# Performance work log

Hardware: AMD Instinct MI355X
Metric: run time of the kernel (lower is better)

Reference implementation:

```python
import jax, jax.numpy as jnp
import numpy as np

ALPHA = 1.0
BETA = 1.0


def setup_inputs() -> dict:
    key = jax.random.key(0)
    k1, k2, k3, k4 = jax.random.split(key, 4)
    B_, S, D_in, D_out, R = 4, 64, 8192, 8192, 16
    x = jax.random.normal(k1, (B_, S, D_in), dtype=jnp.float32)
    original_weight = jax.random.normal(k2, (D_out, D_in), dtype=jnp.float32) * 0.02
    A = jax.random.normal(k3, (D_out, R), dtype=jnp.float32) * 0.02
    Bm = jax.random.normal(k4, (R, D_in), dtype=jnp.float32) * 0.02
    return {"x": x, "original_weight": original_weight, "A": A, "B": Bm}


def reference(x, original_weight, A, B):
    # delta_weight = alpha * (A @ B)  -> [D_out, D_in]
    delta_weight = ALPHA * jnp.matmul(A, B)
    # F.linear(x, W + beta*delta) = x @ (W + beta*delta)^T
    W = original_weight + BETA * delta_weight
    return jnp.einsum("bsd,od->bso", x, W)
```

## Files before the change

kernel.cpp:

```cpp
#include <hip/hip_runtime.h>
#include <stdint.h>


#define DM 256
#define DK 8192
#define DN 8192
#define RLORA 16

#define TN 64
#define BK 64
#define KSPLIT 4
#define KCHUNK (DK / KSPLIT)
#define NITER (KCHUNK / BK)

typedef short bf16x8 __attribute__((ext_vector_type(8)));
typedef float f32x4v __attribute__((ext_vector_type(4)));

__device__ __forceinline__ unsigned short f2bf(float f) {
  unsigned u = __builtin_bit_cast(unsigned, f);
  u += 0x7FFFu + ((u >> 16) & 1u);
  return (unsigned short)(u >> 16);
}

__device__ __forceinline__ bf16x8 pack8(float4 a, float4 b) {
  bf16x8 r;
  r[0] = (short)f2bf(a.x); r[1] = (short)f2bf(a.y);
  r[2] = (short)f2bf(a.z); r[3] = (short)f2bf(a.w);
  r[4] = (short)f2bf(b.x); r[5] = (short)f2bf(b.y);
  r[6] = (short)f2bf(b.z); r[7] = (short)f2bf(b.w);
  return r;
}

__global__ __launch_bounds__(256) void prep_x(
    const float* __restrict__ x, const float* __restrict__ Bm,
    unsigned short* __restrict__ xb, float* __restrict__ y32) {
  const int ks = blockIdx.x;
  const int m0 = blockIdx.y * 4;
  const int t = threadIdx.x;
  const int k = ks * 1024 + t * 4;
  const int K64 = k >> 6, s = (k >> 5) & 1, oct = (k >> 3) & 3;
  const int e = k & 7;
  float4 xv[4];
#pragma unroll
  for (int i = 0; i < 4; ++i) {
    const int m = m0 + i;
    const int g = m >> 4, r = m & 15;
    xv[i] = *(const float4*)(x + (size_t)m * DK + k);
    ushort4 h;
    h.x = f2bf(xv[i].x); h.y = f2bf(xv[i].y);
    h.z = f2bf(xv[i].z); h.w = f2bf(xv[i].w);
    const size_t chunk = (size_t)(K64 * 32 + s * 16 + g) * 64 + oct * 16 + r;
    *(ushort4*)(xb + chunk * 8 + e) = h;
  }
  float acc[4][RLORA];
#pragma unroll
  for (int r = 0; r < RLORA; ++r) {
    float4 b = *(const float4*)(Bm + (size_t)r * DK + k);
#pragma unroll
    for (int i = 0; i < 4; ++i)
      acc[i][r] = xv[i].x * b.x + xv[i].y * b.y + xv[i].z * b.z + xv[i].w * b.w;
  }
#pragma unroll
  for (int off = 32; off >= 1; off >>= 1)
#pragma unroll
    for (int i = 0; i < 4; ++i)
#pragma unroll
      for (int r = 0; r < RLORA; ++r)
        acc[i][r] += __shfl_xor(acc[i][r], off, 64);
  __shared__ float red[4][4][RLORA];
  const int lane = t & 63, wv = t >> 6;
  if (lane == 0) {
#pragma unroll
    for (int i = 0; i < 4; ++i)
#pragma unroll
      for (int r = 0; r < RLORA; ++r) red[wv][i][r] = acc[i][r];
  }
  __syncthreads();
  if (t < 64) {
    int i = t >> 4, r = t & 15;
    float sum = red[0][i][r] + red[1][i][r] + red[2][i][r] + red[3][i][r];
    atomicAdd(y32 + (m0 + i) * RLORA + r, sum);
  }
}

__global__ __launch_bounds__(256) void pack_y(
    const float* __restrict__ y32, unsigned short* __restrict__ yb) {
  int slot = blockIdx.x * 256 + threadIdx.x;
  int fy = slot >> 6, l = slot & 63;
  int oct = l >> 4, r = l & 15;
  int m = fy * 16 + r;
  unsigned short v[8];
#pragma unroll
  for (int e = 0; e < 8; ++e) {
    int c = oct * 8 + e;
    v[e] = (c < RLORA) ? f2bf(y32[m * RLORA + c]) : (unsigned short)0;
  }
  *(ushort4*)(yb + slot * 8) = make_ushort4(v[0], v[1], v[2], v[3]);
  *(ushort4*)(yb + slot * 8 + 4) = make_ushort4(v[4], v[5], v[6], v[7]);
}

__global__ __launch_bounds__(512, 4) void lora_gemm(
    const unsigned short* __restrict__ xb,
    const float* __restrict__ W,
    const unsigned short* __restrict__ yb,
    const float* __restrict__ Aw,
    float* __restrict__ out,
    float* __restrict__ part) {
  __shared__ unsigned short wsm[2][4096];

  const int tid = threadIdx.x;
  const int lane = tid & 63, w = tid >> 6;
  const int mi = w >> 1, ni = w & 1;
  const int qr = lane & 15, quad = lane >> 4;
  const int n0 = blockIdx.x * TN;
  const int kz = blockIdx.y;
  const int kb = kz * KCHUNK;

  const int Fs = w >> 2, Fsub = w & 3;
  const float* wsrc = W + (size_t)(n0 + Fsub * 16 + qr) * DK + kb +
                      Fs * 32 + quad * 8;
  const unsigned wdst = (unsigned)tid * 16;

  const bf16x8* ap = (const bf16x8*)xb + ((size_t)(kz * 32) * 32) * 64 + lane;

  f32x4v acc[4][2];
#pragma unroll
  for (int a = 0; a < 4; ++a)
#pragma unroll
    for (int b = 0; b < 2; ++b) acc[a][b] = (f32x4v){0.f, 0.f, 0.f, 0.f};

  float4 g0 = *(const float4*)(wsrc);
  float4 g1 = *(const float4*)(wsrc + 4);
  *(bf16x8*)((char*)wsm[0] + wdst) = pack8(g0, g1);
  __syncthreads();

  for (int it = 0; it < NITER; ++it) {
    const char* wcur = (const char*)wsm[it & 1];
    char* wnxt = (char*)wsm[(it + 1) & 1];
    const bool havW = (it + 1 < NITER);
    if (havW) {
      const float* p = wsrc + (size_t)(it + 1) * BK;
      g0 = *(const float4*)(p);
      g1 = *(const float4*)(p + 4);
    }
    bf16x8 av[4][2];
#pragma unroll
    for (int s = 0; s < 2; ++s)
#pragma unroll
      for (int mt = 0; mt < 4; ++mt)
        av[mt][s] = ap[(size_t)(s * 16 + mi * 4 + mt) * 64];
    ap += (size_t)32 * 64;
#pragma unroll
    for (int s = 0; s < 2; ++s) {
      bf16x8 b[2];
#pragma unroll
      for (int sub = 0; sub < 2; ++sub)
        b[sub] = *(const bf16x8*)(wcur +
            (((s * 4 + ni * 2 + sub) * 64 + lane) * 16));
#pragma unroll
      for (int mt = 0; mt < 4; ++mt)
#pragma unroll
        for (int sub = 0; sub < 2; ++sub)
          acc[mt][sub] = __builtin_amdgcn_mfma_f32_16x16x32_bf16(
              av[mt][s], b[sub], acc[mt][sub], 0, 0, 0);
    }
    if (havW) *(bf16x8*)(wnxt + wdst) = pack8(g0, g1);
    __syncthreads();
  }

  if (kz == 0) {
    float4 z = {0.f, 0.f, 0.f, 0.f};
    bf16x8 b[2];
#pragma unroll
    for (int sub = 0; sub < 2; ++sub) {
      const float* ap2 = Aw + (size_t)(n0 + ni * 32 + sub * 16 + qr) * RLORA +
                         quad * 8;
      float4 p0 = (quad < 2) ? *(const float4*)(ap2) : z;
      float4 p1 = (quad < 2) ? *(const float4*)(ap2 + 4) : z;
      b[sub] = pack8(p0, p1);
    }
    const bf16x8* yp = (const bf16x8*)yb + lane;
#pragma unroll
    for (int mt = 0; mt < 4; ++mt) {
      bf16x8 av = yp[(size_t)(mi * 4 + mt) * 64];
#pragma unroll
      for (int sub = 0; sub < 2; ++sub)
        acc[mt][sub] = __builtin_amdgcn_mfma_f32_16x16x32_bf16(
            av, b[sub], acc[mt][sub], 0, 0, 0);
    }
  }

  if (part) {
    float* pb = part + (size_t)kz * DM * DN;
#pragma unroll
    for (int mt = 0; mt < 4; ++mt)
#pragma unroll
      for (int sub = 0; sub < 2; ++sub) {
        float* p = pb + (size_t)(mi * 64 + mt * 16 + quad * 4) * DN +
                   n0 + ni * 32 + sub * 16 + qr;
#pragma unroll
        for (int rg = 0; rg < 4; ++rg) p[(size_t)rg * DN] = acc[mt][sub][rg];
      }
  } else {
    float* ob = out;
#pragma unroll
    for (int mt = 0; mt < 4; ++mt)
#pragma unroll
      for (int sub = 0; sub < 2; ++sub) {
        float* p = ob + (size_t)(mi * 64 + mt * 16 + quad * 4) * DN +
                   n0 + ni * 32 + sub * 16 + qr;
#pragma unroll
        for (int rg = 0; rg < 4; ++rg)
          atomicAdd(p + (size_t)rg * DN, acc[mt][sub][rg]);
      }
  }
}

__global__ __launch_bounds__(256) void reduce_k(
    const float* __restrict__ part, float* __restrict__ out) {
  size_t i = ((size_t)blockIdx.x * 256 + threadIdx.x) * 4;
  float4 s = *(const float4*)(part + i);
#pragma unroll
  for (int kzi = 1; kzi < KSPLIT; ++kzi) {
    float4 v = *(const float4*)(part + (size_t)kzi * DM * DN + i);
    s.x += v.x; s.y += v.y; s.z += v.z; s.w += v.w;
  }
  *(float4*)(out + i) = s;
}

extern "C" void kernel_launch(void* const* d_in, const int* in_sizes, int n_in,
                              void* d_out, int out_size, void* d_ws, size_t ws_size,
                              hipStream_t stream) {
  const float* x  = (const float*)d_in[0];
  const float* W  = (const float*)d_in[1];
  const float* A  = (const float*)d_in[2];
  const float* Bm = (const float*)d_in[3];
  float* out = (float*)d_out;

  unsigned short* xb = (unsigned short*)d_ws;
  unsigned short* yb = (unsigned short*)((char*)d_ws + (4u << 20));
  float* y32 = (float*)((char*)yb + 16384);
  size_t base_bytes = (4u << 20) + 16384 + 16384;
  size_t part_bytes = (size_t)KSPLIT * DM * DN * 4;
  bool use_part = ws_size >= base_bytes + part_bytes;
  float* part = use_part ? (float*)((char*)d_ws + base_bytes) : nullptr;

  if (!use_part)
    hipMemsetAsync(d_out, 0, (size_t)out_size * sizeof(float), stream);
  hipMemsetAsync(y32, 0, (size_t)DM * RLORA * sizeof(float), stream);
  prep_x<<<dim3(8, 64), 256, 0, stream>>>(x, Bm, xb, y32);
  pack_y<<<4, 256, 0, stream>>>(y32, yb);
  lora_gemm<<<dim3(DN / TN, KSPLIT), 512, 0, stream>>>(xb, W, yb, A, out, part);
  if (use_part) reduce_k<<<2048, 256, 0, stream>>>(part, out);
}
```

Baseline: 444.8 us.

## Fuse y packing into GEMM, remap blocks to XCDs, retile warps

```diff
diff --git a/kernel.cpp b/kernel.cpp
--- a/kernel.cpp
+++ b/kernel.cpp
@@ -83,26 +83,10 @@
   }
 }
 
-__global__ __launch_bounds__(256) void pack_y(
-    const float* __restrict__ y32, unsigned short* __restrict__ yb) {
-  int slot = blockIdx.x * 256 + threadIdx.x;
-  int fy = slot >> 6, l = slot & 63;
-  int oct = l >> 4, r = l & 15;
-  int m = fy * 16 + r;
-  unsigned short v[8];
-#pragma unroll
-  for (int e = 0; e < 8; ++e) {
-    int c = oct * 8 + e;
-    v[e] = (c < RLORA) ? f2bf(y32[m * RLORA + c]) : (unsigned short)0;
-  }
-  *(ushort4*)(yb + slot * 8) = make_ushort4(v[0], v[1], v[2], v[3]);
-  *(ushort4*)(yb + slot * 8 + 4) = make_ushort4(v[4], v[5], v[6], v[7]);
-}
-
 __global__ __launch_bounds__(512, 4) void lora_gemm(
     const unsigned short* __restrict__ xb,
     const float* __restrict__ W,
-    const unsigned short* __restrict__ yb,
+    const float* __restrict__ y32,
     const float* __restrict__ Aw,
     float* __restrict__ out,
     float* __restrict__ part) {
@@ -110,10 +94,13 @@
 
   const int tid = threadIdx.x;
   const int lane = tid & 63, w = tid >> 6;
-  const int mi = w >> 1, ni = w & 1;
   const int qr = lane & 15, quad = lane >> 4;
-  const int n0 = blockIdx.x * TN;
-  const int kz = blockIdx.y;
+
+  const int bid = blockIdx.x;
+  const int xcd = bid & 7;
+  const int kz = xcd >> 1;
+  const int nblk = (bid >> 3) + ((xcd & 1) << 6);
+  const int n0 = nblk * TN;
   const int kb = kz * KCHUNK;
 
   const int Fs = w >> 2, Fsub = w & 3;
@@ -123,11 +110,11 @@
 
   const bf16x8* ap = (const bf16x8*)xb + ((size_t)(kz * 32) * 32) * 64 + lane;
 
-  f32x4v acc[4][2];
-#pragma unroll
-  for (int a = 0; a < 4; ++a)
-#pragma unroll
-    for (int b = 0; b < 2; ++b) acc[a][b] = (f32x4v){0.f, 0.f, 0.f, 0.f};
+  f32x4v acc[2][4];
+#pragma unroll
+  for (int a = 0; a < 2; ++a)
+#pragma unroll
+    for (int b = 0; b < 4; ++b) acc[a][b] = (f32x4v){0.f, 0.f, 0.f, 0.f};
 
   float4 g0 = *(const float4*)(wsrc);
   float4 g1 = *(const float4*)(wsrc + 4);
@@ -135,80 +122,79 @@
   __syncthreads();
 
   for (int it = 0; it < NITER; ++it) {
-    const char* wcur = (const char*)wsm[it & 1];
-    char* wnxt = (char*)wsm[(it + 1) & 1];
+    bf16x8 av[2][2];
+#pragma unroll
+    for (int s = 0; s < 2; ++s)
+#pragma unroll
+      for (int mt = 0; mt < 2; ++mt)
+        av[mt][s] = ap[(size_t)(s * 16 + w * 2 + mt) * 64];
+    ap += (size_t)32 * 64;
     const bool havW = (it + 1 < NITER);
     if (havW) {
       const float* p = wsrc + (size_t)(it + 1) * BK;
       g0 = *(const float4*)(p);
       g1 = *(const float4*)(p + 4);
     }
-    bf16x8 av[4][2];
-#pragma unroll
-    for (int s = 0; s < 2; ++s)
-#pragma unroll
-      for (int mt = 0; mt < 4; ++mt)
-        av[mt][s] = ap[(size_t)(s * 16 + mi * 4 + mt) * 64];
-    ap += (size_t)32 * 64;
+    const char* wcur = (const char*)wsm[it & 1];
 #pragma unroll
     for (int s = 0; s < 2; ++s) {
-      bf16x8 b[2];
-#pragma unroll
-      for (int sub = 0; sub < 2; ++sub)
-        b[sub] = *(const bf16x8*)(wcur +
-            (((s * 4 + ni * 2 + sub) * 64 + lane) * 16));
-#pragma unroll
-      for (int mt = 0; mt < 4; ++mt)
-#pragma unroll
-        for (int sub = 0; sub < 2; ++sub)
+      bf16x8 b[4];
+#pragma unroll
+      for (int sub = 0; sub < 4; ++sub)
+        b[sub] = *(const bf16x8*)(wcur + (((s * 4 + sub) * 64 + lane) * 16));
+#pragma unroll
+      for (int mt = 0; mt < 2; ++mt)
+#pragma unroll
+        for (int sub = 0; sub < 4; ++sub)
           acc[mt][sub] = __builtin_amdgcn_mfma_f32_16x16x32_bf16(
               av[mt][s], b[sub], acc[mt][sub], 0, 0, 0);
     }
-    if (havW) *(bf16x8*)(wnxt + wdst) = pack8(g0, g1);
+    if (havW) *(bf16x8*)((char*)wsm[(it + 1) & 1] + wdst) = pack8(g0, g1);
     __syncthreads();
   }
 
   if (kz == 0) {
-    float4 z = {0.f, 0.f, 0.f, 0.f};
-    bf16x8 b[2];
-#pragma unroll
-    for (int sub = 0; sub < 2; ++sub) {
-      const float* ap2 = Aw + (size_t)(n0 + ni * 32 + sub * 16 + qr) * RLORA +
-                         quad * 8;
+    const float4 z = {0.f, 0.f, 0.f, 0.f};
+    bf16x8 b[4];
+#pragma unroll
+    for (int sub = 0; sub < 4; ++sub) {
+      const float* ap2 = Aw + (size_t)(n0 + sub * 16 + qr) * RLORA + quad * 8;
       float4 p0 = (quad < 2) ? *(const float4*)(ap2) : z;
       float4 p1 = (quad < 2) ? *(const float4*)(ap2 + 4) : z;
       b[sub] = pack8(p0, p1);
     }
-    const bf16x8* yp = (const bf16x8*)yb + lane;
-#pragma unroll
-    for (int mt = 0; mt < 4; ++mt) {
-      bf16x8 av = yp[(size_t)(mi * 4 + mt) * 64];
-#pragma unroll
-      for (int sub = 0; sub < 2; ++sub)
+#pragma unroll
+    for (int mt = 0; mt < 2; ++mt) {
+      const float* yp = y32 + (size_t)(w * 32 + mt * 16 + qr) * RLORA + quad * 8;
+      float4 q0 = (quad < 2) ? *(const float4*)(yp) : z;
+      float4 q1 = (quad < 2) ? *(const float4*)(yp + 4) : z;
+      bf16x8 avt = pack8(q0, q1);
+#pragma unroll
+      for (int sub = 0; sub < 4; ++sub)
         acc[mt][sub] = __builtin_amdgcn_mfma_f32_16x16x32_bf16(
-            av, b[sub], acc[mt][sub], 0, 0, 0);
+            avt, b[sub], acc[mt][sub], 0, 0, 0);
     }
   }
 
   if (part) {
     float* pb = part + (size_t)kz * DM * DN;
 #pragma unroll
-    for (int mt = 0; mt < 4; ++mt)
-#pragma unroll
-      for (int sub = 0; sub < 2; ++sub) {
-        float* p = pb + (size_t)(mi * 64 + mt * 16 + quad * 4) * DN +
-                   n0 + ni * 32 + sub * 16 + qr;
+    for (int mt = 0; mt < 2; ++mt)
+#pragma unroll
+      for (int sub = 0; sub < 4; ++sub) {
+        float* p = pb + (size_t)(w * 32 + mt * 16 + quad * 4) * DN +
+                   n0 + sub * 16 + qr;
 #pragma unroll
         for (int rg = 0; rg < 4; ++rg) p[(size_t)rg * DN] = acc[mt][sub][rg];
       }
   } else {
     float* ob = out;
 #pragma unroll
-    for (int mt = 0; mt < 4; ++mt)
-#pragma unroll
-      for (int sub = 0; sub < 2; ++sub) {
-        float* p = ob + (size_t)(mi * 64 + mt * 16 + quad * 4) * DN +
-                   n0 + ni * 32 + sub * 16 + qr;
+    for (int mt = 0; mt < 2; ++mt)
+#pragma unroll
+      for (int sub = 0; sub < 4; ++sub) {
+        float* p = ob + (size_t)(w * 32 + mt * 16 + quad * 4) * DN +
+                   n0 + sub * 16 + qr;
 #pragma unroll
         for (int rg = 0; rg < 4; ++rg)
           atomicAdd(p + (size_t)rg * DN, acc[mt][sub][rg]);
@@ -238,9 +224,8 @@
   float* out = (float*)d_out;
 
   unsigned short* xb = (unsigned short*)d_ws;
-  unsigned short* yb = (unsigned short*)((char*)d_ws + (4u << 20));
-  float* y32 = (float*)((char*)yb + 16384);
-  size_t base_bytes = (4u << 20) + 16384 + 16384;
+  float* y32 = (float*)((char*)d_ws + (4u << 20));
+  size_t base_bytes = (4u << 20) + 16384;
   size_t part_bytes = (size_t)KSPLIT * DM * DN * 4;
   bool use_part = ws_size >= base_bytes + part_bytes;
   float* part = use_part ? (float*)((char*)d_ws + base_bytes) : nullptr;
@@ -249,7 +234,6 @@
     hipMemsetAsync(d_out, 0, (size_t)out_size * sizeof(float), stream);
   hipMemsetAsync(y32, 0, (size_t)DM * RLORA * sizeof(float), stream);
   prep_x<<<dim3(8, 64), 256, 0, stream>>>(x, Bm, xb, y32);
-  pack_y<<<4, 256, 0, stream>>>(y32, yb);
-  lora_gemm<<<dim3(DN / TN, KSPLIT), 512, 0, stream>>>(xb, W, yb, A, out, part);
+  lora_gemm<<<512, 512, 0, stream>>>(xb, W, y32, A, out, part);
   if (use_part) reduce_k<<<2048, 256, 0, stream>>>(part, out);
 }
```

After: 425.5 us. 1.05x faster.
